# Optimization experiments

Measured on AMD Instinct MI355X. Metric: run time of the kernel, lower is better.

The kernel has to match this reference:

```python
import jax, jax.numpy as jnp
import numpy as np

VOCAB, HIDDEN, LAYERS, NUM_LABELS, PAD_ID = 32000, 512, 2, 4, 0
B, T = 32, 2048


def setup_inputs() -> dict:
    key = jax.random.key(0)
    ks = jax.random.split(key, 9)
    s = 1.0 / np.sqrt(HIDDEN)
    emb = jax.random.normal(ks[0], (VOCAB, HIDDEN), jnp.float32) * 0.02
    emb = emb.at[PAD_ID].set(0.0)  # padding_idx row is zero
    W_ih = jax.random.uniform(ks[1], (LAYERS, 4 * HIDDEN, HIDDEN), jnp.float32, -s, s)
    W_hh = jax.random.uniform(ks[2], (LAYERS, 4 * HIDDEN, HIDDEN), jnp.float32, -s, s)
    b_ih = jax.random.uniform(ks[3], (LAYERS, 4 * HIDDEN), jnp.float32, -s, s)
    b_hh = jax.random.uniform(ks[4], (LAYERS, 4 * HIDDEN), jnp.float32, -s, s)
    fc_w = jax.random.uniform(ks[5], (NUM_LABELS, HIDDEN), jnp.float32, -s, s)
    fc_b = jax.random.uniform(ks[6], (NUM_LABELS,), jnp.float32, -s, s)
    x = jax.random.randint(ks[7], (B, T), 0, VOCAB)
    labels = jax.random.randint(ks[8], (B,), 0, NUM_LABELS)
    return {"x": x, "labels": labels, "emb": emb, "W_ih": W_ih, "W_hh": W_hh,
            "b_ih": b_ih, "b_hh": b_hh, "fc_w": fc_w, "fc_b": fc_b}


def _lstm_layer(xs_tbh, Wih, Whh, bih, bhh):
    # xs_tbh: [T, B, H] time-major. PyTorch gate order: i, f, g, o.
    Bsz = xs_tbh.shape[1]
    H = Whh.shape[1]
    ix = jnp.einsum('tbh,gh->tbg', xs_tbh, Wih) + bih + bhh  # precompute input proj

    def step(carry, ix_t):
        h, c = carry
        gates = ix_t + h @ Whh.T  # [B, 4H]
        i, f, g, o = jnp.split(gates, 4, axis=-1)
        c = jax.nn.sigmoid(f) * c + jax.nn.sigmoid(i) * jnp.tanh(g)
        h = jax.nn.sigmoid(o) * jnp.tanh(c)
        return (h, c), h

    h0 = jnp.zeros((Bsz, H), xs_tbh.dtype)
    (hT, cT), hs = jax.lax.scan(step, (h0, h0), ix)
    return hs, hT, cT


def reference(x, labels, emb, W_ih, W_hh, b_ih, b_hh, fc_w, fc_b):
    h = emb[x]                      # [B, T, H] embedding lookup
    hs = jnp.transpose(h, (1, 0, 2))  # [T, B, H]
    for l in range(W_ih.shape[0]):  # small fixed layer loop
        hs, hT, _ = _lstm_layer(hs, W_ih[l], W_hh[l], b_ih[l], b_hh[l])
    logits = hT @ fc_w.T + fc_b     # [B, num_labels]
    logp = jax.nn.log_softmax(logits, axis=-1)
    loss = -jnp.take_along_axis(logp, labels[:, None], axis=-1).mean()
    return loss, logits
```

## Files before the change

### kernel.cpp

```cpp
#include <hip/hip_runtime.h>
#include <stdint.h>

#define TSEQ 2048
#define BATCH 32
#define HID 512
#define NWG_ALL 128

typedef _Float16 half8 __attribute__((ext_vector_type(8)));
typedef float floatx4 __attribute__((ext_vector_type(4)));

__device__ __forceinline__ float sigf(float x){ return 1.f/(1.f+__expf(-x)); }
__device__ __forceinline__ float tanh_(float x){
  float e = __expf(-2.f*fabsf(x));
  float r = (1.f-e)/(1.f+e);
  return x<0.f ? -r : r;
}
__device__ __forceinline__ half8 cvt8(float4 a, float4 b){
  return half8{(_Float16)a.x,(_Float16)a.y,(_Float16)a.z,(_Float16)a.w,
               (_Float16)b.x,(_Float16)b.y,(_Float16)b.z,(_Float16)b.w};
}
__device__ __forceinline__ half8 ldh8_coh(const _Float16* p){
  const unsigned long long* q = (const unsigned long long*)p;
  unsigned long long a = __hip_atomic_load(q,   __ATOMIC_RELAXED, __HIP_MEMORY_SCOPE_AGENT);
  unsigned long long b = __hip_atomic_load(q+1, __ATOMIC_RELAXED, __HIP_MEMORY_SCOPE_AGENT);
  union { unsigned long long u[2]; half8 h; } v; v.u[0]=a; v.u[1]=b; return v.h;
}

__global__ void k_cvt_emb(const float* __restrict__ in, _Float16* __restrict__ out, int n8){
  int i = blockIdx.x*256 + threadIdx.x;
  if (i < n8){
    const float4* s = (const float4*)(in + (size_t)i*8);
    *(half8*)(out + (size_t)i*8) = cvt8(s[0], s[1]);
  }
}

__global__ void __launch_bounds__(256,1) k_main(
    const int* __restrict__ xtok, const _Float16* __restrict__ emb16,
    const float* __restrict__ Wih, const float* __restrict__ Whh,
    const float* __restrict__ bih, const float* __restrict__ bhh,
    _Float16* __restrict__ h0ring, _Float16* __restrict__ h1ring,
    float* __restrict__ hT, unsigned* __restrict__ flags){
  int tid = threadIdx.x, lane = tid&63, wave = tid>>6;
  int wgAll = blockIdx.x, layer = wgAll>>6, wg = wgAll&63;
  int mh = wave>>1, nh = wave&1;
  int kg = lane>>4, r15 = lane&15;
  int bcol = nh*16 + r15;
  int u = mh*4 + kg;

  half8 wx[16], wh[16];
  {
    int m = mh*16 + r15;
    int grow = ((m&3)<<9) + (wg<<3) + (m>>2);
    const float* pwx = Wih + ((size_t)layer*2048 + grow)*HID + kg*8;
    const float* pwh = Whh + ((size_t)layer*2048 + grow)*HID + kg*8;
    #pragma unroll
    for (int ks=0; ks<16; ++ks){
      wx[ks] = cvt8(*(const float4*)(pwx + ks*32), *(const float4*)(pwx + ks*32 + 4));
      wh[ks] = cvt8(*(const float4*)(pwh + ks*32), *(const float4*)(pwh + ks*32 + 4));
    }
  }
  float bias[4];
  #pragma unroll
  for (int r=0; r<4; ++r){
    int g = layer*2048 + (r<<9) + (wg<<3) + u;
    bias[r] = bih[g] + bhh[g];
  }

  unsigned* myring32 = (unsigned*)(layer ? h1ring : h0ring);
  const _Float16* hring = layer ? h1ring : h0ring;

  floatx4 accx = {bias[0], bias[1], bias[2], bias[3]};
  if (layer == 0){
    int tok = xtok[bcol*TSEQ + 0];
    const _Float16* px = emb16 + (size_t)tok*HID + kg*8;
    #pragma unroll
    for (int ks=0; ks<16; ++ks){
      half8 xf = *(const half8*)(px + ks*32);
      accx = __builtin_amdgcn_mfma_f32_16x16x32_f16(wx[ks], xf, accx, 0,0,0);
    }
  }

  float c_st = 0.f;
  for (int tt=0; tt<=TSEQ+1; ++tt){
    bool act = (layer==0) ? (tt < TSEQ) : (tt >= 2);
    int t = (layer==0) ? tt : tt-2;
    if (act){
      floatx4 acc = accx;
      if (t > 0){
        const _Float16* hb = hring + (size_t)((t-1)&7)*(BATCH*HID) + bcol*HID + kg*8;
        half8 hf[16];
        #pragma unroll
        for (int ks=0; ks<16; ++ks) hf[ks] = ldh8_coh(hb + ks*32);
        #pragma unroll
        for (int ks=0; ks<16; ++ks)
          acc = __builtin_amdgcn_mfma_f32_16x16x32_f16(wh[ks], hf[ks], acc, 0,0,0);
      }
      float gi = acc[0], gf = acc[1], gg = acc[2], go = acc[3];
      c_st = sigf(gf)*c_st + sigf(gi)*tanh_(gg);
      float h = sigf(go)*tanh_(c_st);
      unsigned short hb16; { _Float16 hh = (_Float16)h; __builtin_memcpy(&hb16, &hh, 2); }
      unsigned partner = __shfl_down((unsigned)hb16, 16);
      if ((kg & 1) == 0)
        __hip_atomic_store(&myring32[ ((((t&7)*BATCH + bcol)*HID + (wg<<3) + u) >> 1) ],
                           (unsigned)hb16 | (partner << 16),
                           __ATOMIC_RELAXED, __HIP_MEMORY_SCOPE_AGENT);
      if (layer==1 && t==TSEQ-1) hT[bcol*HID + (wg<<3) + u] = h;
    }
    __syncthreads();
    if (tid == 0)
      __hip_atomic_store(&flags[wgAll], (unsigned)(tt+1),
                         __ATOMIC_RELAXED, __HIP_MEMORY_SCOPE_AGENT);
    int ntt = tt+1;
    bool nact = (layer==0) ? (ntt < TSEQ) : (ntt >= 2 && ntt <= TSEQ+1);
    if (nact){
      accx = floatx4{bias[0], bias[1], bias[2], bias[3]};
      half8 xf[16];
      if (layer == 0){
        int tok = xtok[bcol*TSEQ + ntt];
        const _Float16* px = emb16 + (size_t)tok*HID + kg*8;
        #pragma unroll
        for (int ks=0; ks<16; ++ks) xf[ks] = *(const half8*)(px + ks*32);
      } else {
        const _Float16* px = h0ring + (size_t)((ntt-2)&7)*(BATCH*HID) + bcol*HID + kg*8;
        #pragma unroll
        for (int ks=0; ks<16; ++ks) xf[ks] = ldh8_coh(px + ks*32);
      }
      #pragma unroll
      for (int ks=0; ks<16; ++ks)
        accx = __builtin_amdgcn_mfma_f32_16x16x32_f16(wx[ks], xf[ks], accx, 0,0,0);
    }
    if (tt <= TSEQ){
      if (wave == 0){
        unsigned tgt = (unsigned)(tt+1);
        for (;;){
          unsigned f0 = __hip_atomic_load(&flags[lane],    __ATOMIC_RELAXED, __HIP_MEMORY_SCOPE_AGENT);
          unsigned f1 = __hip_atomic_load(&flags[64+lane], __ATOMIC_RELAXED, __HIP_MEMORY_SCOPE_AGENT);
          if (__all(f0 >= tgt && f1 >= tgt)) break;
          __builtin_amdgcn_s_sleep(2);
        }
      }
      __syncthreads();
    }
  }
}

__global__ void k_cls(const float* __restrict__ hT, const float* __restrict__ fcw,
                      const float* __restrict__ fcb, const int* __restrict__ labels,
                      float* __restrict__ out){
  __shared__ float lg[128];
  __shared__ float ls[32];
  int tid = threadIdx.x;
  if (tid < 128){
    int b = tid>>2, n = tid&3;
    const float4* hp = (const float4*)(hT + b*HID);
    const float4* wp = (const float4*)(fcw + n*HID);
    float s = 0.f;
    for (int k=0;k<128;++k){ float4 a = hp[k], w = wp[k];
      s += a.x*w.x + a.y*w.y + a.z*w.z + a.w*w.w; }
    lg[tid] = s + fcb[n];
  }
  __syncthreads();
  if (tid < 32){
    float x0 = lg[tid*4+0], x1 = lg[tid*4+1], x2 = lg[tid*4+2], x3 = lg[tid*4+3];
    float mx = fmaxf(fmaxf(x0,x1),fmaxf(x2,x3));
    float lse = mx + logf(__expf(x0-mx)+__expf(x1-mx)+__expf(x2-mx)+__expf(x3-mx));
    ls[tid] = lse - lg[tid*4 + labels[tid]];
  }
  __syncthreads();
  if (tid == 0){
    float s = 0.f;
    for (int b=0;b<32;++b) s += ls[b];
    out[0] = s * (1.f/32.f);
  }
  if (tid < 128) out[1+tid] = lg[tid];
}

extern "C" void kernel_launch(void* const* d_in, const int* in_sizes, int n_in,
                              void* d_out, int out_size, void* d_ws, size_t ws_size,
                              hipStream_t stream) {
  const int*   x      = (const int*)d_in[0];
  const int*   labels = (const int*)d_in[1];
  const float* emb    = (const float*)d_in[2];
  const float* Wih    = (const float*)d_in[3];
  const float* Whh    = (const float*)d_in[4];
  const float* bih    = (const float*)d_in[5];
  const float* bhh    = (const float*)d_in[6];
  const float* fcw    = (const float*)d_in[7];
  const float* fcb    = (const float*)d_in[8];
  float* out = (float*)d_out;
  char* ws = (char*)d_ws;

  _Float16* emb16  = (_Float16*)(ws);
  _Float16* h0ring = (_Float16*)(ws + (32ull<<20));
  _Float16* h1ring = (_Float16*)(ws + (32ull<<20) + (256<<10));
  float*    hT     = (float*)   (ws + (32ull<<20) + (512<<10));
  unsigned* flags  = (unsigned*)(ws + (32ull<<20) + (576<<10));

  hipMemsetAsync(flags, 0, 1024, stream);
  k_cvt_emb<<<8000, 256, 0, stream>>>(emb, emb16, 2048000);
  k_main<<<NWG_ALL, 256, 0, stream>>>(x, emb16, Wih, Whh, bih, bhh,
                                      h0ring, h1ring, hT, flags);
  k_cls<<<1, 256, 0, stream>>>(hT, fcw, fcb, labels, out);
}
```

Before: 17.80 ms.

## Shrink persistent LSTM grid to 32 workgroups of 8 waves with blocked h layout

Reduces the persistent kernel from 128 workgroups of 4 waves to 32 workgroups of 8 waves. Each wave now owns 16 gate rows for the full 32-column batch, done as two MFMA column tiles. The hidden-state ring is stored in a k-blocked layout so the B-operand loads are contiguous. Every wave now polls the flags directly instead of wave 0 polling followed by a barrier. The aim is a cheaper per-step grid barrier with fewer participants and less sync overhead, at the cost of twice the per-wave serial MFMA and load work on the recurrent critical path.

New measurement: 25.82 ms. 1.45x slower.

```diff
diff --git a/kernel.cpp b/kernel.cpp
--- a/kernel.cpp
+++ b/kernel.cpp
@@ -4,7 +4,8 @@
 #define TSEQ 2048
 #define BATCH 32
 #define HID 512
-#define NWG_ALL 128
+#define NWGL 16
+#define NWG_ALL 32
 
 typedef _Float16 half8 __attribute__((ext_vector_type(8)));
 typedef float floatx4 __attribute__((ext_vector_type(4)));
@@ -34,23 +35,20 @@
   }
 }
 
-__global__ void __launch_bounds__(256,1) k_main(
+__global__ void __launch_bounds__(512,1) k_main(
     const int* __restrict__ xtok, const _Float16* __restrict__ emb16,
     const float* __restrict__ Wih, const float* __restrict__ Whh,
     const float* __restrict__ bih, const float* __restrict__ bhh,
     _Float16* __restrict__ h0ring, _Float16* __restrict__ h1ring,
     float* __restrict__ hT, unsigned* __restrict__ flags){
   int tid = threadIdx.x, lane = tid&63, wave = tid>>6;
-  int wgAll = blockIdx.x, layer = wgAll>>6, wg = wgAll&63;
-  int mh = wave>>1, nh = wave&1;
+  int wgAll = blockIdx.x, layer = wgAll>>4, wg = wgAll&15;
   int kg = lane>>4, r15 = lane&15;
-  int bcol = nh*16 + r15;
-  int u = mh*4 + kg;
 
   half8 wx[16], wh[16];
   {
-    int m = mh*16 + r15;
-    int grow = ((m&3)<<9) + (wg<<3) + (m>>2);
+    int m = wave*16 + r15;
+    int grow = ((m&3)<<9) + (wg<<5) + (m>>2);
     const float* pwx = Wih + ((size_t)layer*2048 + grow)*HID + kg*8;
     const float* pwh = Whh + ((size_t)layer*2048 + grow)*HID + kg*8;
     #pragma unroll
@@ -59,52 +57,76 @@
       wh[ks] = cvt8(*(const float4*)(pwh + ks*32), *(const float4*)(pwh + ks*32 + 4));
     }
   }
+  int u = wave*4 + kg;
+  int j = (wg<<5) + u;
   float bias[4];
   #pragma unroll
   for (int r=0; r<4; ++r){
-    int g = layer*2048 + (r<<9) + (wg<<3) + u;
+    int g = layer*2048 + (r<<9) + (wg<<5) + u;
     bias[r] = bih[g] + bhh[g];
   }
 
-  unsigned* myring32 = (unsigned*)(layer ? h1ring : h0ring);
+  unsigned* ring32 = (unsigned*)(layer ? h1ring : h0ring);
   const _Float16* hring = layer ? h1ring : h0ring;
-
-  floatx4 accx = {bias[0], bias[1], bias[2], bias[3]};
+  int stElemBase = ((j>>3)*32)*8 + (j&7);
+
+  floatx4 accx0 = {bias[0],bias[1],bias[2],bias[3]};
+  floatx4 accx1 = accx0;
   if (layer == 0){
-    int tok = xtok[bcol*TSEQ + 0];
-    const _Float16* px = emb16 + (size_t)tok*HID + kg*8;
     #pragma unroll
-    for (int ks=0; ks<16; ++ks){
-      half8 xf = *(const half8*)(px + ks*32);
-      accx = __builtin_amdgcn_mfma_f32_16x16x32_f16(wx[ks], xf, accx, 0,0,0);
-    }
-  }
-
-  float c_st = 0.f;
+    for (int nt=0; nt<2; ++nt){
+      int tok = xtok[(nt*16+r15)*TSEQ + 0];
+      const _Float16* px = emb16 + (size_t)tok*HID + kg*8;
+      floatx4 a = nt ? accx1 : accx0;
+      #pragma unroll
+      for (int ks=0; ks<16; ++ks){
+        half8 xf = *(const half8*)(px + ks*32);
+        a = __builtin_amdgcn_mfma_f32_16x16x32_f16(wx[ks], xf, a, 0,0,0);
+      }
+      if (nt) accx1 = a; else accx0 = a;
+    }
+  }
+
+  float c0 = 0.f, c1 = 0.f;
   for (int tt=0; tt<=TSEQ+1; ++tt){
     bool act = (layer==0) ? (tt < TSEQ) : (tt >= 2);
     int t = (layer==0) ? tt : tt-2;
     if (act){
-      floatx4 acc = accx;
+      floatx4 acc0 = accx0, acc1 = accx1;
       if (t > 0){
-        const _Float16* hb = hring + (size_t)((t-1)&7)*(BATCH*HID) + bcol*HID + kg*8;
-        half8 hf[16];
+        const _Float16* hb = hring + (size_t)((t-1)&7)*(BATCH*HID);
         #pragma unroll
-        for (int ks=0; ks<16; ++ks) hf[ks] = ldh8_coh(hb + ks*32);
-        #pragma unroll
-        for (int ks=0; ks<16; ++ks)
-          acc = __builtin_amdgcn_mfma_f32_16x16x32_f16(wh[ks], hf[ks], acc, 0,0,0);
-      }
-      float gi = acc[0], gf = acc[1], gg = acc[2], go = acc[3];
-      c_st = sigf(gf)*c_st + sigf(gi)*tanh_(gg);
-      float h = sigf(go)*tanh_(c_st);
-      unsigned short hb16; { _Float16 hh = (_Float16)h; __builtin_memcpy(&hb16, &hh, 2); }
-      unsigned partner = __shfl_down((unsigned)hb16, 16);
-      if ((kg & 1) == 0)
-        __hip_atomic_store(&myring32[ ((((t&7)*BATCH + bcol)*HID + (wg<<3) + u) >> 1) ],
-                           (unsigned)hb16 | (partner << 16),
-                           __ATOMIC_RELAXED, __HIP_MEMORY_SCOPE_AGENT);
-      if (layer==1 && t==TSEQ-1) hT[bcol*HID + (wg<<3) + u] = h;
+        for (int nt=0; nt<2; ++nt){
+          half8 hf[16];
+          #pragma unroll
+          for (int ks=0; ks<16; ++ks)
+            hf[ks] = ldh8_coh(hb + (((ks*4+kg)*32 + nt*16 + r15)<<3));
+          floatx4 a = nt ? acc1 : acc0;
+          #pragma unroll
+          for (int ks=0; ks<16; ++ks)
+            a = __builtin_amdgcn_mfma_f32_16x16x32_f16(wh[ks], hf[ks], a, 0,0,0);
+          if (nt) acc1 = a; else acc0 = a;
+        }
+      }
+      c0 = sigf(acc0[1])*c0 + sigf(acc0[0])*tanh_(acc0[2]);
+      float h0v = sigf(acc0[3])*tanh_(c0);
+      c1 = sigf(acc1[1])*c1 + sigf(acc1[0])*tanh_(acc1[2]);
+      float h1v = sigf(acc1[3])*tanh_(c1);
+      size_t slotBase = (size_t)(t&7)*(BATCH*HID);
+      unsigned b0, b1;
+      { _Float16 hh = (_Float16)h0v; unsigned short s; __builtin_memcpy(&s,&hh,2); b0 = s; }
+      { _Float16 hh = (_Float16)h1v; unsigned short s; __builtin_memcpy(&s,&hh,2); b1 = s; }
+      unsigned p0 = __shfl_down(b0, 16), p1 = __shfl_down(b1, 16);
+      if ((kg & 1) == 0){
+        __hip_atomic_store(&ring32[(slotBase + stElemBase + (size_t)(r15)*8)>>1],
+                           b0 | (p0<<16), __ATOMIC_RELAXED, __HIP_MEMORY_SCOPE_AGENT);
+        __hip_atomic_store(&ring32[(slotBase + stElemBase + (size_t)(16+r15)*8)>>1],
+                           b1 | (p1<<16), __ATOMIC_RELAXED, __HIP_MEMORY_SCOPE_AGENT);
+      }
+      if (layer==1 && t==TSEQ-1){
+        hT[(r15)*HID + j] = h0v;
+        hT[(16+r15)*HID + j] = h1v;
+      }
     }
     __syncthreads();
     if (tid == 0)
@@ -113,33 +135,38 @@
     int ntt = tt+1;
     bool nact = (layer==0) ? (ntt < TSEQ) : (ntt >= 2 && ntt <= TSEQ+1);
     if (nact){
-      accx = floatx4{bias[0], bias[1], bias[2], bias[3]};
-      half8 xf[16];
-      if (layer == 0){
-        int tok = xtok[bcol*TSEQ + ntt];
-        const _Float16* px = emb16 + (size_t)tok*HID + kg*8;
+      accx0 = floatx4{bias[0],bias[1],bias[2],bias[3]};
+      accx1 = accx0;
+      #pragma unroll
+      for (int nt=0; nt<2; ++nt){
+        half8 xf[16];
+        if (layer == 0){
+          int tok = xtok[(nt*16+r15)*TSEQ + ntt];
+          const _Float16* px = emb16 + (size_t)tok*HID + kg*8;
+          #pragma unroll
+          for (int ks=0; ks<16; ++ks) xf[ks] = *(const half8*)(px + ks*32);
+        } else {
+          const _Float16* px = h0ring + (size_t)((ntt-2)&7)*(BATCH*HID);
+          #pragma unroll
+          for (int ks=0; ks<16; ++ks)
+            xf[ks] = ldh8_coh(px + (((ks*4+kg)*32 + nt*16 + r15)<<3));
+        }
+        floatx4 a = nt ? accx1 : accx0;
         #pragma unroll
-        for (int ks=0; ks<16; ++ks) xf[ks] = *(const half8*)(px + ks*32);
-      } else {
-        const _Float16* px = h0ring + (size_t)((ntt-2)&7)*(BATCH*HID) + bcol*HID + kg*8;
-        #pragma unroll
-        for (int ks=0; ks<16; ++ks) xf[ks] = ldh8_coh(px + ks*32);
-      }
-      #pragma unroll
-      for (int ks=0; ks<16; ++ks)
-        accx = __builtin_amdgcn_mfma_f32_16x16x32_f16(wx[ks], xf[ks], accx, 0,0,0);
+        for (int ks=0; ks<16; ++ks)
+          a = __builtin_amdgcn_mfma_f32_16x16x32_f16(wx[ks], xf[ks], a, 0,0,0);
+        if (nt) accx1 = a; else accx0 = a;
+      }
     }
     if (tt <= TSEQ){
-      if (wave == 0){
-        unsigned tgt = (unsigned)(tt+1);
-        for (;;){
-          unsigned f0 = __hip_atomic_load(&flags[lane],    __ATOMIC_RELAXED, __HIP_MEMORY_SCOPE_AGENT);
-          unsigned f1 = __hip_atomic_load(&flags[64+lane], __ATOMIC_RELAXED, __HIP_MEMORY_SCOPE_AGENT);
-          if (__all(f0 >= tgt && f1 >= tgt)) break;
-          __builtin_amdgcn_s_sleep(2);
-        }
-      }
-      __syncthreads();
+      unsigned tgt = (unsigned)(tt+1);
+      for (;;){
+        unsigned f = tgt;
+        if (lane < NWG_ALL)
+          f = __hip_atomic_load(&flags[lane], __ATOMIC_RELAXED, __HIP_MEMORY_SCOPE_AGENT);
+        if (__all(f >= tgt)) break;
+        __builtin_amdgcn_s_sleep(2);
+      }
     }
   }
 }
@@ -198,7 +225,7 @@
 
   hipMemsetAsync(flags, 0, 1024, stream);
   k_cvt_emb<<<8000, 256, 0, stream>>>(emb, emb16, 2048000);
-  k_main<<<NWG_ALL, 256, 0, stream>>>(x, emb16, Wih, Whh, bih, bhh,
+  k_main<<<NWG_ALL, 512, 0, stream>>>(x, emb16, Wih, Whh, bih, bhh,
                                       h0ring, h1ring, hT, flags);
   k_cls<<<1, 256, 0, stream>>>(hT, fcw, fcb, labels, out);
 }
```
